# Performance work log

Hardware: AMD Instinct MI355X
Metric: run time of the kernel (lower is better)

The kernel has to match this reference:

```python
import jax, jax.numpy as jnp
import numpy as np

B, T, C, H = 4, 2048, 1024, 16
D = C // H  # head_dim = 64


def setup_inputs() -> dict:
    key = jax.random.key(0)
    ks = jax.random.split(key, 5)
    s = 0.02
    return {
        "x": jax.random.normal(ks[0], (B, T, C), dtype=jnp.float32),
        "w_qkv": jax.random.normal(ks[1], (C, 3 * C), dtype=jnp.float32) * s,
        "b_qkv": jnp.zeros((3 * C,), dtype=jnp.float32),
        "w_proj": jax.random.normal(ks[2], (C, C), dtype=jnp.float32) * s,
        "b_proj": jnp.zeros((C,), dtype=jnp.float32),
    }


def reference(x, w_qkv, b_qkv, w_proj, b_proj):
    Bx, Tx, Cx = x.shape
    qkv = x @ w_qkv + b_qkv                      # [B,T,3C]
    q, k, v = jnp.split(qkv, 3, axis=-1)
    # [B,T,C] -> [B,H,T,D]
    q = q.reshape(Bx, Tx, H, D).transpose(0, 2, 1, 3)
    k = k.reshape(Bx, Tx, H, D).transpose(0, 2, 1, 3)
    v = v.reshape(Bx, Tx, H, D).transpose(0, 2, 1, 3)
    scale = 1.0 / np.sqrt(D).astype(np.float32)
    attn = jnp.einsum('bhqd,bhkd->bhqk', q, k) * scale   # [B,H,T,T]
    causal = jnp.tril(jnp.ones((Tx, Tx), dtype=bool))
    attn = jnp.where(causal[None, None], attn, -jnp.inf)
    attn = jax.nn.softmax(attn, axis=-1)
    out = jnp.einsum('bhqk,bhkd->bhqd', attn, v)          # [B,H,T,D]
    out = out.transpose(0, 2, 1, 3).reshape(Bx, Tx, Cx)   # [B,T,C]
    return out @ w_proj + b_proj
```

## Files before the change

### kernel.cpp

```cpp
#include <hip/hip_runtime.h>
#include <hip/hip_bf16.h>
#include <math.h>

using bf16 = __hip_bfloat16;
typedef __bf16 bf16x8 __attribute__((ext_vector_type(8)));
typedef float  f32x4  __attribute__((ext_vector_type(4)));
typedef unsigned short ushort8 __attribute__((ext_vector_type(8)));

#define DEV __device__ __forceinline__

DEV void gld_lds16(const void* g, void* l) {
    __builtin_amdgcn_global_load_lds((const __attribute__((address_space(1))) void*)g,
                                     (__attribute__((address_space(3))) void*)l,
                                     16, 0, 0);
}

__global__ __launch_bounds__(256) void cast_f32_bf16(const float* __restrict__ in,
                                                     bf16* __restrict__ out, int n4) {
    int i = blockIdx.x * blockDim.x + threadIdx.x;
    if (i >= n4) return;
    float4 f = ((const float4*)in)[i];
    __align__(8) bf16 o[4] = {__float2bfloat16(f.x), __float2bfloat16(f.y),
                              __float2bfloat16(f.z), __float2bfloat16(f.w)};
    ((uint64_t*)out)[i] = *(const uint64_t*)o;
}

__global__ __launch_bounds__(256) void transpose_cast(const float* __restrict__ in,
                                                      bf16* __restrict__ out, int R, int Cn) {
    __shared__ float tile[32][33];
    int bx = blockIdx.x * 32;
    int by = blockIdx.y * 32;
    int tx = threadIdx.x & 31, ty = threadIdx.x >> 5;
    for (int i = ty; i < 32; i += 8)
        tile[i][tx] = in[(size_t)(by + i) * Cn + bx + tx];
    __syncthreads();
    for (int i = ty; i < 32; i += 8)
        out[(size_t)(bx + i) * R + by + tx] = __float2bfloat16(tile[tx][i]);
}

__global__ __launch_bounds__(256) void transpose_v(const bf16* __restrict__ in,
                                                   bf16* __restrict__ out) {
    __shared__ bf16 tile[64][72];
    int bh = blockIdx.y;
    int t0 = blockIdx.x * 64;
    const bf16* ib = in + (size_t)bh * 2048 * 64 + (size_t)t0 * 64;
    bf16* ob = out + (size_t)bh * 64 * 2048 + t0;
    int r = threadIdx.x >> 2, c = (threadIdx.x & 3) * 16;
    *(ushort8*)&tile[r][c]     = *(const ushort8*)(ib + (size_t)r * 64 + c);
    *(ushort8*)&tile[r][c + 8] = *(const ushort8*)(ib + (size_t)r * 64 + c + 8);
    __syncthreads();
    int d = threadIdx.x >> 2, t = (threadIdx.x & 3) * 16;
    __align__(16) bf16 tmp[16];
    for (int j = 0; j < 16; ++j) tmp[j] = tile[t + j][d];
    *(ushort8*)(ob + (size_t)d * 2048 + t)     = *(const ushort8*)tmp;
    *(ushort8*)(ob + (size_t)d * 2048 + t + 8) = *(const ushort8*)(tmp + 8);
}

__global__ __launch_bounds__(256) void gemm_qkv(const bf16* __restrict__ A,
                                                const bf16* __restrict__ Bt,
                                                const float* __restrict__ bias,
                                                bf16* __restrict__ qb,
                                                bf16* __restrict__ kb,
                                                bf16* __restrict__ vb) {
    constexpr int K = 1024, T = 2048;
    constexpr float CS = 0.18033688f;
    __shared__ __align__(16) bf16 Al[128 * 32];
    __shared__ __align__(16) bf16 Bl[128 * 32];
    int tid = threadIdx.x;
    int lane = tid & 63, w = tid >> 6;
    int wm = w >> 1, wn = w & 1;
    int l15 = lane & 15, quad = lane >> 4;
    int m0 = blockIdx.x * 128, n0 = blockIdx.y * 128;

    f32x4 acc[4][4] = {};
    for (int k0 = 0; k0 < K; k0 += 32) {
        __syncthreads();
        for (int it = 0; it < 2; ++it) {
            int e = (it * 256 + tid) * 8;
            int r = e >> 5, c = e & 31;
            gld_lds16(A  + (size_t)(m0 + r) * K + k0 + c, &Al[e]);
            gld_lds16(Bt + (size_t)(n0 + r) * K + k0 + c, &Bl[e]);
        }
        __syncthreads();
        bf16x8 af[4], bfr[4];
        for (int i = 0; i < 4; ++i)
            af[i] = *(const bf16x8*)&Al[(wm * 64 + i * 16 + l15) * 32 + quad * 8];
        for (int j = 0; j < 4; ++j)
            bfr[j] = *(const bf16x8*)&Bl[(wn * 64 + j * 16 + l15) * 32 + quad * 8];
        for (int i = 0; i < 4; ++i)
            for (int j = 0; j < 4; ++j)
                acc[i][j] = __builtin_amdgcn_mfma_f32_16x16x32_bf16(af[i], bfr[j], acc[i][j], 0, 0, 0);
    }
    for (int i = 0; i < 4; ++i) {
        int mbase = m0 + wm * 64 + i * 16 + quad * 4;
        for (int j = 0; j < 4; ++j) {
            int n = n0 + wn * 64 + j * 16 + l15;
            float bv = bias[n];
            for (int v = 0; v < 4; ++v) {
                int mm = mbase + v;
                int b = mm >> 11, t = mm & 2047;
                float val = acc[i][j][v] + bv;
                if (n < 1024) {
                    int h = n >> 6, d = n & 63;
                    qb[(((size_t)(b * 16 + h)) * T + t) * 64 + d] = __float2bfloat16(val * CS);
                } else if (n < 2048) {
                    int n2 = n - 1024; int h = n2 >> 6, d = n2 & 63;
                    kb[(((size_t)(b * 16 + h)) * T + t) * 64 + d] = __float2bfloat16(val);
                } else {
                    int n2 = n - 2048; int h = n2 >> 6, d = n2 & 63;
                    vb[(((size_t)(b * 16 + h)) * T + t) * 64 + d] = __float2bfloat16(val);
                }
            }
        }
    }
}

__global__ __launch_bounds__(256, 4) void flash_attn(const bf16* __restrict__ qb,
                                                     const bf16* __restrict__ kbuf,
                                                     const bf16* __restrict__ vT,
                                                     bf16* __restrict__ ob) {
    constexpr int T = 2048;
    __shared__ __align__(16) bf16 Kl[64 * 64];
    __shared__ __align__(16) bf16 Vl[64 * 64];
    __shared__ __align__(16) bf16 Pl[4 * 2 * 16 * 72];
    int tid = threadIdx.x;
    int lane = tid & 63, w = tid >> 6;
    int l15 = lane & 15, quad = lane >> 4;

    int g = blockIdx.x;
    int quarter = g >> 8;
    int j = (g >> 6) & 3;
    int bh = g & 63;
    int xq;
    switch (quarter) {
        case 0:  xq = 15 - j; break;
        case 1:  xq = 8 + j;  break;
        case 2:  xq = 4 + j;  break;
        default: xq = 3 - j;  break;
    }
    int q0 = xq << 7;
    const bf16* qbase = qb   + (size_t)bh * T * 64;
    const bf16* kbase = kbuf + (size_t)bh * T * 64;
    const bf16* vbase = vT   + (size_t)bh * 64 * T;

    int qg[2];
    bf16x8 qa[2][2];
    for (int s = 0; s < 2; ++s) {
        qg[s] = q0 + w * 32 + s * 16 + l15;
        for (int c = 0; c < 2; ++c)
            qa[s][c] = *(const bf16x8*)(qbase + (size_t)qg[s] * 64 + c * 32 + quad * 8);
    }

    bf16x8 ones;
    for (int i = 0; i < 8; ++i) ones[i] = (__bf16)1.0f;

    f32x4 O[2][4] = {};
    f32x4 O1[2] = {};
    int h7 = l15 & 7;

    int nit = 2 * xq + 2;
    for (int t = 0; t < nit; ++t) {
        int kb = t << 6;
        __syncthreads();
        for (int it = 0; it < 2; ++it) {
            int off = (it * 256 + tid) * 8;
            int r = off >> 6, cb = (off >> 3) & 7;
            gld_lds16(kbase + (size_t)(kb + r) * 64 + ((cb ^ (r & 7)) << 3), &Kl[off]);
            gld_lds16(vbase + (size_t)r * T + kb + ((cb ^ (r & 7)) << 3), &Vl[off]);
        }
        __syncthreads();

        bool maskt = (t >= nit - 2);
        for (int jn = 0; jn < 4; ++jn) {
            int row = jn * 16 + l15;
            bf16x8 a0 = *(const bf16x8*)&Kl[row * 64 + ((quad ^ h7) << 3)];
            bf16x8 a1 = *(const bf16x8*)&Kl[row * 64 + (((4 + quad) ^ h7) << 3)];
            f32x4 sa[2] = {};
            for (int s = 0; s < 2; ++s) {
                sa[s] = __builtin_amdgcn_mfma_f32_16x16x32_bf16(a0, qa[s][0], sa[s], 0, 0, 0);
                sa[s] = __builtin_amdgcn_mfma_f32_16x16x32_bf16(a1, qa[s][1], sa[s], 0, 0, 0);
            }
            for (int s = 0; s < 2; ++s) {
                __align__(8) bf16 pb[4];
                for (int v = 0; v < 4; ++v) {
                    float p = exp2f(sa[s][v]);
                    if (maskt) {
                        int key = kb + jn * 16 + quad * 4 + v;
                        p = (key <= qg[s]) ? p : 0.f;
                    }
                    pb[v] = __float2bfloat16(p);
                }
                *(uint64_t*)&Pl[((w * 2 + s) * 16 + l15) * 72 + jn * 16 + quad * 4] =
                    *(const uint64_t*)pb;
            }
        }
        asm volatile("s_waitcnt lgkmcnt(0)" ::: "memory");
        bf16x8 pf[2][2];
        for (int s = 0; s < 2; ++s) {
            for (int c = 0; c < 2; ++c)
                pf[s][c] = *(const bf16x8*)&Pl[((w * 2 + s) * 16 + l15) * 72 + c * 32 + quad * 8];
            O1[s] = __builtin_amdgcn_mfma_f32_16x16x32_bf16(pf[s][0], ones, O1[s], 0, 0, 0);
            O1[s] = __builtin_amdgcn_mfma_f32_16x16x32_bf16(pf[s][1], ones, O1[s], 0, 0, 0);
        }
        for (int jd = 0; jd < 4; ++jd) {
            int vrow = jd * 16 + l15;
            bf16x8 v0 = *(const bf16x8*)&Vl[vrow * 64 + ((quad ^ h7) << 3)];
            bf16x8 v1 = *(const bf16x8*)&Vl[vrow * 64 + (((4 + quad) ^ h7) << 3)];
            O[0][jd] = __builtin_amdgcn_mfma_f32_16x16x32_bf16(pf[0][0], v0, O[0][jd], 0, 0, 0);
            O[0][jd] = __builtin_amdgcn_mfma_f32_16x16x32_bf16(pf[0][1], v1, O[0][jd], 0, 0, 0);
            O[1][jd] = __builtin_amdgcn_mfma_f32_16x16x32_bf16(pf[1][0], v0, O[1][jd], 0, 0, 0);
            O[1][jd] = __builtin_amdgcn_mfma_f32_16x16x32_bf16(pf[1][1], v1, O[1][jd], 0, 0, 0);
        }
    }

    int b = bh >> 4, h = bh & 15;
    for (int s = 0; s < 2; ++s) {
        float linv[4];
        for (int v = 0; v < 4; ++v) linv[v] = 1.f / O1[s][v];
        for (int jd = 0; jd < 4; ++jd) {
            for (int v = 0; v < 4; ++v) {
                int qr = q0 + w * 32 + s * 16 + quad * 4 + v;
                ob[((size_t)(b * T + qr)) * 1024 + h * 64 + jd * 16 + l15] =
                    __float2bfloat16(O[s][jd][v] * linv[v]);
            }
        }
    }
}

__global__ __launch_bounds__(256) void gemm_proj(const bf16* __restrict__ A,
                                                 const bf16* __restrict__ Bt,
                                                 const float* __restrict__ bias,
                                                 float* __restrict__ out) {
    constexpr int K = 1024, N = 1024;
    __shared__ __align__(16) bf16 Al[128 * 32];
    __shared__ __align__(16) bf16 Bl[128 * 32];
    int tid = threadIdx.x;
    int lane = tid & 63, w = tid >> 6;
    int wm = w >> 1, wn = w & 1;
    int l15 = lane & 15, quad = lane >> 4;
    int m0 = blockIdx.x * 128, n0 = blockIdx.y * 128;

    f32x4 acc[4][4] = {};
    for (int k0 = 0; k0 < K; k0 += 32) {
        __syncthreads();
        for (int it = 0; it < 2; ++it) {
            int e = (it * 256 + tid) * 8;
            int r = e >> 5, c = e & 31;
            gld_lds16(A  + (size_t)(m0 + r) * K + k0 + c, &Al[e]);
            gld_lds16(Bt + (size_t)(n0 + r) * K + k0 + c, &Bl[e]);
        }
        __syncthreads();
        bf16x8 af[4], bfr[4];
        for (int i = 0; i < 4; ++i)
            af[i] = *(const bf16x8*)&Al[(wm * 64 + i * 16 + l15) * 32 + quad * 8];
        for (int j = 0; j < 4; ++j)
            bfr[j] = *(const bf16x8*)&Bl[(wn * 64 + j * 16 + l15) * 32 + quad * 8];
        for (int i = 0; i < 4; ++i)
            for (int j = 0; j < 4; ++j)
                acc[i][j] = __builtin_amdgcn_mfma_f32_16x16x32_bf16(af[i], bfr[j], acc[i][j], 0, 0, 0);
    }
    for (int i = 0; i < 4; ++i) {
        int mbase = m0 + wm * 64 + i * 16 + quad * 4;
        for (int j = 0; j < 4; ++j) {
            int n = n0 + wn * 64 + j * 16 + l15;
            float bv = bias[n];
            for (int v = 0; v < 4; ++v)
                out[(size_t)(mbase + v) * N + n] = acc[i][j][v] + bv;
        }
    }
}

extern "C" void kernel_launch(void* const* d_in, const int* in_sizes, int n_in,
                              void* d_out, int out_size, void* d_ws, size_t ws_size,
                              hipStream_t stream) {
    (void)in_sizes; (void)n_in; (void)out_size; (void)ws_size;
    const float* x      = (const float*)d_in[0];
    const float* w_qkv  = (const float*)d_in[1];
    const float* b_qkv  = (const float*)d_in[2];
    const float* w_proj = (const float*)d_in[3];
    const float* b_proj = (const float*)d_in[4];
    float* out = (float*)d_out;

    char* ws = (char*)d_ws;
    bf16* xb     = (bf16*)(ws);
    bf16* wqkvT  = (bf16*)(ws + (16u << 20));
    bf16* wprojT = (bf16*)(ws + (22u << 20));
    bf16* qbuf   = (bf16*)(ws + (24u << 20));
    bf16* kbuf   = (bf16*)(ws + (40u << 20));
    bf16* vb     = (bf16*)(ws + (56u << 20));
    bf16* vTb    = (bf16*)(ws + (72u << 20));
    bf16* ob     = (bf16*)(ws + (56u << 20));

    cast_f32_bf16<<<8192, 256, 0, stream>>>(x, xb, 8192 * 1024 / 4);
    transpose_cast<<<dim3(3072 / 32, 1024 / 32), 256, 0, stream>>>(w_qkv, wqkvT, 1024, 3072);
    transpose_cast<<<dim3(1024 / 32, 1024 / 32), 256, 0, stream>>>(w_proj, wprojT, 1024, 1024);
    gemm_qkv<<<dim3(64, 24), 256, 0, stream>>>(xb, wqkvT, b_qkv, qbuf, kbuf, vb);
    transpose_v<<<dim3(32, 64), 256, 0, stream>>>(vb, vTb);
    flash_attn<<<1024, 256, 0, stream>>>(qbuf, kbuf, vTb, ob);
    gemm_proj<<<dim3(64, 8), 256, 0, stream>>>(ob, wprojT, b_proj, out);
}
```

Measured before the change: 281.5 us.

## Fuse V transpose into QKV GEMM epilogue via LDS staging

The QKV GEMM epilogue now stages each 16-row slice of output in shared memory, then writes Q and K with 16-byte vector stores and writes V directly in transposed [b,h,d,t] layout. This removes the separate transpose_v kernel launch and its extra read/write of the V tensor, and replaces scattered 2-byte stores with coalesced vector stores. The cost is extra LDS use and syncthreads in the epilogue, which may reduce occupancy slightly.

```diff
diff --git a/kernel.cpp b/kernel.cpp
--- a/kernel.cpp
+++ b/kernel.cpp
@@ -38,34 +38,17 @@
         out[(size_t)(bx + i) * R + by + tx] = __float2bfloat16(tile[tx][i]);
 }
 
-__global__ __launch_bounds__(256) void transpose_v(const bf16* __restrict__ in,
-                                                   bf16* __restrict__ out) {
-    __shared__ bf16 tile[64][72];
-    int bh = blockIdx.y;
-    int t0 = blockIdx.x * 64;
-    const bf16* ib = in + (size_t)bh * 2048 * 64 + (size_t)t0 * 64;
-    bf16* ob = out + (size_t)bh * 64 * 2048 + t0;
-    int r = threadIdx.x >> 2, c = (threadIdx.x & 3) * 16;
-    *(ushort8*)&tile[r][c]     = *(const ushort8*)(ib + (size_t)r * 64 + c);
-    *(ushort8*)&tile[r][c + 8] = *(const ushort8*)(ib + (size_t)r * 64 + c + 8);
-    __syncthreads();
-    int d = threadIdx.x >> 2, t = (threadIdx.x & 3) * 16;
-    __align__(16) bf16 tmp[16];
-    for (int j = 0; j < 16; ++j) tmp[j] = tile[t + j][d];
-    *(ushort8*)(ob + (size_t)d * 2048 + t)     = *(const ushort8*)tmp;
-    *(ushort8*)(ob + (size_t)d * 2048 + t + 8) = *(const ushort8*)(tmp + 8);
-}
-
 __global__ __launch_bounds__(256) void gemm_qkv(const bf16* __restrict__ A,
                                                 const bf16* __restrict__ Bt,
                                                 const float* __restrict__ bias,
                                                 bf16* __restrict__ qb,
                                                 bf16* __restrict__ kb,
-                                                bf16* __restrict__ vb) {
+                                                bf16* __restrict__ vTb) {
     constexpr int K = 1024, T = 2048;
     constexpr float CS = 0.18033688f;
     __shared__ __align__(16) bf16 Al[128 * 32];
     __shared__ __align__(16) bf16 Bl[128 * 32];
+    __shared__ __align__(16) bf16 Et[32 * 136];
     int tid = threadIdx.x;
     int lane = tid & 63, w = tid >> 6;
     int wm = w >> 1, wn = w & 1;
@@ -91,26 +74,43 @@
             for (int j = 0; j < 4; ++j)
                 acc[i][j] = __builtin_amdgcn_mfma_f32_16x16x32_bf16(af[i], bfr[j], acc[i][j], 0, 0, 0);
     }
+
+    int mode = (blockIdx.y < 8) ? 0 : (blockIdx.y < 16 ? 1 : 2);
+    float bv[4];
+    for (int j = 0; j < 4; ++j)
+        bv[j] = bias[n0 + wn * 64 + j * 16 + l15];
+    float scl = (mode == 0) ? CS : 1.0f;
+
     for (int i = 0; i < 4; ++i) {
-        int mbase = m0 + wm * 64 + i * 16 + quad * 4;
-        for (int j = 0; j < 4; ++j) {
-            int n = n0 + wn * 64 + j * 16 + l15;
-            float bv = bias[n];
-            for (int v = 0; v < 4; ++v) {
-                int mm = mbase + v;
-                int b = mm >> 11, t = mm & 2047;
-                float val = acc[i][j][v] + bv;
-                if (n < 1024) {
-                    int h = n >> 6, d = n & 63;
-                    qb[(((size_t)(b * 16 + h)) * T + t) * 64 + d] = __float2bfloat16(val * CS);
-                } else if (n < 2048) {
-                    int n2 = n - 1024; int h = n2 >> 6, d = n2 & 63;
-                    kb[(((size_t)(b * 16 + h)) * T + t) * 64 + d] = __float2bfloat16(val);
-                } else {
-                    int n2 = n - 2048; int h = n2 >> 6, d = n2 & 63;
-                    vb[(((size_t)(b * 16 + h)) * T + t) * 64 + d] = __float2bfloat16(val);
-                }
-            }
+        __syncthreads();
+        for (int j = 0; j < 4; ++j)
+            for (int v = 0; v < 4; ++v)
+                Et[(wm * 16 + quad * 4 + v) * 136 + wn * 64 + j * 16 + l15] =
+                    __float2bfloat16((acc[i][j][v] + bv[j]) * scl);
+        __syncthreads();
+        if (mode < 2) {
+            int r = tid >> 3, cc = (tid & 7) * 16;
+            int m = m0 + i * 16 + (r < 16 ? r : r + 48);
+            int b = m >> 11, t = m & 2047;
+            int n = (n0 & 1023) + cc;
+            int h = n >> 6, d = n & 63;
+            bf16* dst = (mode == 0 ? qb : kb) + (((size_t)(b * 16 + h)) * T + t) * 64 + d;
+            ushort8 u0 = *(const ushort8*)&Et[r * 136 + cc];
+            ushort8 u1 = *(const ushort8*)&Et[r * 136 + cc + 8];
+            *(ushort8*)dst = u0;
+            *(ushort8*)(dst + 8) = u1;
+        } else {
+            int run = tid >> 7, d = tid & 127;
+            int t0 = m0 + i * 16 + run * 64;
+            int b = t0 >> 11, tt = t0 & 2047;
+            int n = (n0 & 1023) + d;
+            int h = n >> 6, dd = n & 63;
+            __align__(16) bf16 tmp[16];
+            for (int jj = 0; jj < 16; ++jj)
+                tmp[jj] = Et[(run * 16 + jj) * 136 + d];
+            bf16* dst = vTb + (((size_t)(b * 16 + h)) * 64 + dd) * T + tt;
+            *(ushort8*)dst = *(const ushort8*)tmp;
+            *(ushort8*)(dst + 8) = *(const ushort8*)(tmp + 8);
         }
     }
 }
@@ -287,15 +287,13 @@
     bf16* wprojT = (bf16*)(ws + (22u << 20));
     bf16* qbuf   = (bf16*)(ws + (24u << 20));
     bf16* kbuf   = (bf16*)(ws + (40u << 20));
-    bf16* vb     = (bf16*)(ws + (56u << 20));
     bf16* vTb    = (bf16*)(ws + (72u << 20));
     bf16* ob     = (bf16*)(ws + (56u << 20));
 
     cast_f32_bf16<<<8192, 256, 0, stream>>>(x, xb, 8192 * 1024 / 4);
     transpose_cast<<<dim3(3072 / 32, 1024 / 32), 256, 0, stream>>>(w_qkv, wqkvT, 1024, 3072);
     transpose_cast<<<dim3(1024 / 32, 1024 / 32), 256, 0, stream>>>(w_proj, wprojT, 1024, 1024);
-    gemm_qkv<<<dim3(64, 24), 256, 0, stream>>>(xb, wqkvT, b_qkv, qbuf, kbuf, vb);
-    transpose_v<<<dim3(32, 64), 256, 0, stream>>>(vb, vTb);
+    gemm_qkv<<<dim3(64, 24), 256, 0, stream>>>(xb, wqkvT, b_qkv, qbuf, kbuf, vTb);
     flash_attn<<<1024, 256, 0, stream>>>(qbuf, kbuf, vTb, ob);
     gemm_proj<<<dim3(64, 8), 256, 0, stream>>>(ob, wprojT, b_proj, out);
 }
```

Measured after the change: 261.6 us. 1.08x faster.
